# Performance work log

Hardware: AMD Instinct MI355X
Metric: run time of the kernel (lower is better)

## Reference

```python
import jax, jax.numpy as jnp
import numpy as np

DIM = 512        # model dim
MOE_DIM = 256    # expert hidden dim
E = 64           # n_routed experts
G = 8            # n_routed_group
TOPK_G = 4       # n_topk_group
K = 8            # n_experts_per_tok
SCALE = 2.5      # routed_scale
CAP = 1024


def setup_inputs() -> dict:
    key = jax.random.key(0)
    ks = jax.random.split(key, 6)
    x = jax.random.normal(ks[0], (4, 512, DIM), jnp.float32)
    gate_w = jax.random.normal(ks[1], (E, DIM), jnp.float32) / np.sqrt(DIM).astype(np.float32)
    gate_b = jax.random.normal(ks[2], (E,), jnp.float32) * 0.01
    w1 = jax.random.normal(ks[3], (E, DIM, MOE_DIM), jnp.float32) / np.sqrt(DIM).astype(np.float32)
    w3 = jax.random.normal(ks[4], (E, DIM, MOE_DIM), jnp.float32) / np.sqrt(DIM).astype(np.float32)
    w2 = jax.random.normal(ks[5], (E, MOE_DIM, DIM), jnp.float32) / np.sqrt(MOE_DIM).astype(np.float32)
    return {"x": x, "gate_w": gate_w, "gate_b": gate_b, "w1": w1, "w3": w3, "w2": w2}


def _gate(x2, gate_w, gate_b):
    # x2: [T, DIM] -> (weights [T,K], indices [T,K])
    T = x2.shape[0]
    scores = jax.nn.sigmoid(x2 @ gate_w.T)                      # [T, E]
    s = (scores + gate_b).reshape(T, G, E // G)                  # grouped scores
    group_scores = jax.lax.top_k(s, 2)[0].sum(-1)                # [T, G] sum of top-2 per group
    top_groups = jax.lax.top_k(group_scores, TOPK_G)[1]          # [T, TOPK_G]
    gmask = jnp.zeros((T, G), bool).at[jnp.arange(T)[:, None], top_groups].set(True)
    s = jnp.where(gmask[..., None], s, -jnp.inf).reshape(T, E)
    idx = jax.lax.top_k(s, K)[1]                                 # [T, K]
    w = jnp.take_along_axis(scores, idx, axis=1)                 # original (pre-bias) scores
    w = w / w.sum(-1, keepdims=True) * SCALE
    return w, idx


def _moe_forward(x, gate_w, gate_b, w1, w3, w2):
    shape = x.shape
    x2 = x.reshape(-1, DIM)                                      # [T, DIM]
    T = x2.shape[0]
    w, idx = _gate(x2, gate_w, gate_b)
    flat_e = idx.reshape(-1)                                     # [T*K]
    # position of each (token, slot) within its expert's buffer, in order
    oh = (flat_e[:, None] == jnp.arange(E)[None, :]).astype(jnp.int32)  # [T*K, E]
    pos = (jnp.cumsum(oh, axis=0) * oh).sum(-1) - 1              # [T*K]
    x_rep = jnp.repeat(x2, K, axis=0)                            # [T*K, DIM]
    # dispatch into per-expert buffers [E, CAP, DIM]
    xb = jnp.zeros((E, CAP, DIM), x2.dtype).at[flat_e, pos].set(x_rep, mode='drop')
    h = jax.nn.silu(jnp.einsum('ecd,edm->ecm', xb, w1)) * jnp.einsum('ecd,edm->ecm', xb, w3)
    yb = jnp.einsum('ecm,emd->ecd', h, w2)                       # [E, CAP, DIM]
    # combine: gather back and weight
    y = yb.at[flat_e, pos].get(mode='fill', fill_value=0.0) * w.reshape(-1)[:, None]
    return y.reshape(T, K, DIM).sum(1).reshape(shape)


def reference(x, gate_w, gate_b, w1, w3, w2):
    return _moe_forward(x, gate_w, gate_b, w1, w3, w2)
```

## Files before the change

kernel.cpp:

```cpp
#include <hip/hip_runtime.h>

#define T_TOK 2048
#define DIM   512
#define MOE   256
#define NE    64
#define NG    8
#define TOPKG 4
#define TOPK  8
#define CAP   1024
#define MOE_SCALE 2.5f

typedef float f32x4 __attribute__((ext_vector_type(4)));
typedef short s16x8 __attribute__((ext_vector_type(8)));

__device__ __forceinline__ unsigned short f2bf(float f) {
    unsigned u = __builtin_bit_cast(unsigned, f);
    unsigned r = (u + 0x7fffu + ((u >> 16) & 1u)) >> 16;
    return (unsigned short)r;
}
__device__ __forceinline__ unsigned pk2(float lo, float hi) {
    return (unsigned)f2bf(lo) | ((unsigned)f2bf(hi) << 16);
}

__device__ __forceinline__ void tile_scan(const int* __restrict__ counts, int lane,
                                          int e, int& G0, int& ne, int& nt)
{
    int cl = min(counts[lane], CAP);
    int ntl = (cl + 31) >> 5;
    int v = ntl;
#pragma unroll
    for (int d = 1; d < 64; d <<= 1) {
        int o = __shfl_up(v, d);
        if (lane >= d) v += o;
    }
    G0 = __shfl(v - ntl, e);
    ne = __shfl(cl, e);
    nt = __shfl(ntl, e);
}

__global__ __launch_bounds__(256) void gwt_k(const float* __restrict__ gw,
                                             float* __restrict__ gwT)
{
    int idx = blockIdx.x * 256 + threadIdx.x;
    int e = idx >> 9, k = idx & 511;
    gwT[(size_t)(k >> 2) * 256 + e * 4 + (k & 3)] = gw[idx];
}

__global__ __launch_bounds__(256) void gate_fused_k(const float* __restrict__ x,
                                                    const float* __restrict__ gwT,
                                                    const float* __restrict__ gb,
                                                    int* __restrict__ counts,
                                                    int* __restrict__ etok,
                                                    float* __restrict__ wt_of,
                                                    short* __restrict__ xb)
{
    __shared__ float xs[4][512];
    __shared__ float ps[4][4][64];
    int w = threadIdx.x >> 6, lane = threadIdx.x & 63;
    int t = blockIdx.x * 4 + w;

    {
        const float4* xr = (const float4*)(x + (size_t)t * DIM);
        float4 v0 = xr[lane * 2], v1 = xr[lane * 2 + 1];
        *(float4*)&xs[w][lane * 8]     = v0;
        *(float4*)&xs[w][lane * 8 + 4] = v1;
        short o[8];
        o[0] = (short)f2bf(v0.x); o[1] = (short)f2bf(v0.y);
        o[2] = (short)f2bf(v0.z); o[3] = (short)f2bf(v0.w);
        o[4] = (short)f2bf(v1.x); o[5] = (short)f2bf(v1.y);
        o[6] = (short)f2bf(v1.z); o[7] = (short)f2bf(v1.w);
        *(s16x8*)(xb + (size_t)t * DIM + lane * 8) = *(const s16x8*)o;
    }
    __syncthreads();

    const f32x4* gt = (const f32x4*)gwT;
    float a0 = 0.f, a1 = 0.f, a2 = 0.f, a3 = 0.f;
    int kb = w * 32;
#pragma unroll 8
    for (int k4 = 0; k4 < 32; ++k4) {
        f32x4 g  = gt[(size_t)(kb + k4) * 64 + lane];
        f32x4 x0 = *(const f32x4*)&xs[0][(kb + k4) * 4];
        f32x4 x1 = *(const f32x4*)&xs[1][(kb + k4) * 4];
        f32x4 x2 = *(const f32x4*)&xs[2][(kb + k4) * 4];
        f32x4 x3 = *(const f32x4*)&xs[3][(kb + k4) * 4];
        a0 += g.x * x0.x + g.y * x0.y + g.z * x0.z + g.w * x0.w;
        a1 += g.x * x1.x + g.y * x1.y + g.z * x1.z + g.w * x1.w;
        a2 += g.x * x2.x + g.y * x2.y + g.z * x2.z + g.w * x2.w;
        a3 += g.x * x3.x + g.y * x3.y + g.z * x3.z + g.w * x3.w;
    }
    ps[w][0][lane] = a0; ps[w][1][lane] = a1;
    ps[w][2][lane] = a2; ps[w][3][lane] = a3;
    __syncthreads();
    float acc = ps[0][w][lane] + ps[1][w][lane] + ps[2][w][lane] + ps[3][w][lane];

    float sc = 1.f / (1.f + __expf(-acc));
    float s  = sc + gb[lane];

    float m1 = s, m2 = -1e30f;
#pragma unroll
    for (int d = 1; d < 8; d <<= 1) {
        float o1 = __shfl_xor(m1, d);
        float o2 = __shfl_xor(m2, d);
        float n1 = fmaxf(m1, o1);
        float n2 = fmaxf(fminf(m1, o1), fmaxf(m2, o2));
        m1 = n1; m2 = n2;
    }
    float gv = m1 + m2;

    bool gkeep = false;
#pragma unroll
    for (int it = 0; it < TOPKG; ++it) {
        float m = gv;
#pragma unroll
        for (int d = 1; d < 64; d <<= 1) m = fmaxf(m, __shfl_xor(m, d));
        unsigned long long mask = __ballot(gv == m);
        int ldr = __ffsll(mask) - 1;
        if ((lane >> 3) == (ldr >> 3)) { gkeep = true; gv = -2e30f; }
    }
    float sv = gkeep ? s : -1e30f;

    float wsum = 0.f;
    int my_e = 0; float my_w = 0.f;
#pragma unroll
    for (int k = 0; k < TOPK; ++k) {
        float m = sv;
#pragma unroll
        for (int d = 1; d < 64; d <<= 1) m = fmaxf(m, __shfl_xor(m, d));
        unsigned long long mask = __ballot(sv == m);
        int l = __ffsll(mask) - 1;
        float wk = __shfl(sc, l);
        wsum += wk;
        if (lane == k) { my_e = l; my_w = wk; }
        if (lane == l) sv = -2e30f;
    }
    float scale = MOE_SCALE / wsum;
    if (lane < TOPK) {
        int p = atomicAdd(&counts[my_e], 1);
        int rid = t * TOPK + lane;
        bool ok = (p < CAP);
        if (ok) etok[my_e * CAP + p] = rid;
        wt_of[rid] = ok ? my_w * scale : 0.f;
    }
}

__global__ __launch_bounds__(256) void dispatch_k(const short* __restrict__ xb,
                                                  const int* __restrict__ counts,
                                                  const int* __restrict__ etok,
                                                  short* __restrict__ xg)
{
    int e = blockIdx.x & 63, sub = blockIdx.x >> 6;
    int w = threadIdx.x >> 6, lane = threadIdx.x & 63;

    int G0, ne, nt;
    tile_scan(counts, lane, e, G0, ne, nt);
    int rows = nt * 32;
    const int* el = etok + e * CAP;

    int kt = lane >> 2, qq = lane & 3;
    for (int p = sub * 4 + w; p < rows; p += 32) {
        s16x8 v = {0, 0, 0, 0, 0, 0, 0, 0};
        if (p < ne) {
            int tok = el[p] >> 3;
            v = *(const s16x8*)(xb + (size_t)tok * DIM + lane * 8);
        }
        int st = (p >> 4) & 1, m = p & 15;
        size_t off = ((((size_t)(G0 + (p >> 5)) * 16 + kt) * 2 + st) * 64
                      + (qq * 16 + m)) * 8;
        *(s16x8*)(xg + off) = v;
    }
}

__global__ __launch_bounds__(256, 3) void gemm1_k(const short* __restrict__ xg,
                                                  const float* __restrict__ w1,
                                                  const float* __restrict__ w3,
                                                  const int* __restrict__ counts,
                                                  short* __restrict__ hgf)
{
    __shared__ short Bl[2][16][64][8];
    __shared__ short Ct[4][2][16][24];

    int e  = blockIdx.x & 63, cg = blockIdx.x >> 6;
    int n0 = cg * 16;
    int tid = threadIdx.x;
    int w = tid >> 6, lane = tid & 63;
    int q = lane >> 4, m16 = lane & 15;

    int G0, ne, nt;
    tile_scan(counts, lane, e, G0, ne, nt);
    (void)ne;

    const float* W1e = w1 + (size_t)e * DIM * MOE + n0;
    const float* W3e = w3 + (size_t)e * DIM * MOE + n0;
#pragma unroll 4
    for (int it = 0; it < 8; ++it) {
        int idx = it * 256 + tid;
        int mat = idx >> 10;
        int rem = idx & 1023;
        int r2  = rem >> 2;
        int cq  = (rem & 3) * 4;
        int k   = r2 * 2;
        int kt = k >> 5, qf = (k >> 3) & 3, j0 = k & 7;
        const float* p = (mat ? W3e : W1e) + (size_t)k * MOE + cq;
        f32x4 lo = __builtin_nontemporal_load((const f32x4*)p);
        f32x4 hi = __builtin_nontemporal_load((const f32x4*)(p + MOE));
        unsigned* b = (unsigned*)&Bl[mat][kt][qf * 16 + cq][j0];
        b[0]  = pk2(lo.x, hi.x);
        b[4]  = pk2(lo.y, hi.y);
        b[8]  = pk2(lo.z, hi.z);
        b[12] = pk2(lo.w, hi.w);
    }
    __syncthreads();

    for (int T = w; T < nt; T += 4) {
        const short* A = xg + (size_t)(G0 + T) * 16384 + lane * 8;

        f32x4 acc[2][2];
#pragma unroll
        for (int i = 0; i < 2; ++i)
#pragma unroll
            for (int j = 0; j < 2; ++j) acc[i][j] = (f32x4)0.f;

        s16x8 pa0[2], pa1[2];
#pragma unroll
        for (int i = 0; i < 2; ++i) {
            pa0[i] = *(const s16x8*)(A + (i * 2 + 0) * 512);
            pa1[i] = *(const s16x8*)(A + (i * 2 + 1) * 512);
        }
#pragma unroll
        for (int kt = 0; kt < 16; ++kt) {
            s16x8 a0 = pa0[kt & 1], a1 = pa1[kt & 1];
            if (kt < 14) {
                pa0[kt & 1] = *(const s16x8*)(A + ((kt + 2) * 2 + 0) * 512);
                pa1[kt & 1] = *(const s16x8*)(A + ((kt + 2) * 2 + 1) * 512);
            }
            s16x8 b1 = *(const s16x8*)&Bl[0][kt][lane][0];
            s16x8 b3 = *(const s16x8*)&Bl[1][kt][lane][0];
            acc[0][0] = __builtin_amdgcn_mfma_f32_16x16x32_bf16(a0, b1, acc[0][0], 0, 0, 0);
            acc[1][0] = __builtin_amdgcn_mfma_f32_16x16x32_bf16(a1, b1, acc[1][0], 0, 0, 0);
            acc[0][1] = __builtin_amdgcn_mfma_f32_16x16x32_bf16(a0, b3, acc[0][1], 0, 0, 0);
            acc[1][1] = __builtin_amdgcn_mfma_f32_16x16x32_bf16(a1, b3, acc[1][1], 0, 0, 0);
        }

#pragma unroll
        for (int sub = 0; sub < 2; ++sub)
#pragma unroll
            for (int r = 0; r < 4; ++r) {
                float g = acc[sub][0][r];
                float u = acc[sub][1][r];
                float hv = g / (1.f + __expf(-g)) * u;
                Ct[w][sub][q * 4 + r][m16] = (short)f2bf(hv);
            }
        int subr = q >> 1;
        s16x8 hv8 = *(const s16x8*)&Ct[w][subr][m16][(q & 1) * 8];
        size_t slot = ((size_t)(G0 + T) * 8 + (cg >> 1)) * 2 + subr;
        *(s16x8*)(hgf + slot * 512 + ((cg & 1) * 2 + (q & 1)) * 128 + m16 * 8) = hv8;
    }
}

__global__ __launch_bounds__(256, 3) void gemm2_k(const short* __restrict__ hgf,
                                                  const float* __restrict__ w2,
                                                  const int* __restrict__ counts,
                                                  const int* __restrict__ etok,
                                                  short* __restrict__ ybuf)
{
    __shared__ short Bl[2][8][64][8];

    int e  = blockIdx.x & 63, cg = blockIdx.x >> 6;
    int n0 = cg * 32;
    int tid = threadIdx.x;
    int w = tid >> 6, lane = tid & 63;
    int q = lane >> 4, m16 = lane & 15;

    int G0, ne, nt;
    tile_scan(counts, lane, e, G0, ne, nt);

    const float* W2e = w2 + (size_t)e * MOE * DIM + n0;
#pragma unroll 4
    for (int it = 0; it < 4; ++it) {
        int idx = it * 256 + tid;
        int r2  = idx >> 3;
        int cq  = (idx & 7) * 4;
        int k   = r2 * 2;
        int kt2 = k >> 5, qf = (k >> 3) & 3, j0 = k & 7;
        int s = cq >> 4, c15 = cq & 15;
        const float* p = W2e + (size_t)k * DIM + cq;
        f32x4 lo = __builtin_nontemporal_load((const f32x4*)p);
        f32x4 hi = __builtin_nontemporal_load((const f32x4*)(p + DIM));
        unsigned* b = (unsigned*)&Bl[s][kt2][qf * 16 + c15][j0];
        b[0]  = pk2(lo.x, hi.x);
        b[4]  = pk2(lo.y, hi.y);
        b[8]  = pk2(lo.z, hi.z);
        b[12] = pk2(lo.w, hi.w);
    }
    __syncthreads();

    const int* el = etok + e * CAP;

    for (int T = w; T < nt; T += 4) {
        const short* A = hgf + (size_t)(G0 + T) * 8192 + lane * 8;

        int erid[2][4];
#pragma unroll
        for (int sub = 0; sub < 2; ++sub)
#pragma unroll
            for (int r = 0; r < 4; ++r) {
                int row = T * 32 + sub * 16 + q * 4 + r;
                erid[sub][r] = row < ne ? el[row] : -1;
            }

        f32x4 acc[2][2];
#pragma unroll
        for (int i = 0; i < 2; ++i)
#pragma unroll
            for (int j = 0; j < 2; ++j) acc[i][j] = (f32x4)0.f;

        s16x8 pa0[2], pa1[2];
#pragma unroll
        for (int i = 0; i < 2; ++i) {
            pa0[i] = *(const s16x8*)(A + (i * 2 + 0) * 512);
            pa1[i] = *(const s16x8*)(A + (i * 2 + 1) * 512);
        }
#pragma unroll
        for (int kt = 0; kt < 8; ++kt) {
            s16x8 a0 = pa0[kt & 1], a1 = pa1[kt & 1];
            if (kt < 6) {
                pa0[kt & 1] = *(const s16x8*)(A + ((kt + 2) * 2 + 0) * 512);
                pa1[kt & 1] = *(const s16x8*)(A + ((kt + 2) * 2 + 1) * 512);
            }
            s16x8 b0 = *(const s16x8*)&Bl[0][kt][lane][0];
            s16x8 b1 = *(const s16x8*)&Bl[1][kt][lane][0];
            acc[0][0] = __builtin_amdgcn_mfma_f32_16x16x32_bf16(a0, b0, acc[0][0], 0, 0, 0);
            acc[1][0] = __builtin_amdgcn_mfma_f32_16x16x32_bf16(a1, b0, acc[1][0], 0, 0, 0);
            acc[0][1] = __builtin_amdgcn_mfma_f32_16x16x32_bf16(a0, b1, acc[0][1], 0, 0, 0);
            acc[1][1] = __builtin_amdgcn_mfma_f32_16x16x32_bf16(a1, b1, acc[1][1], 0, 0, 0);
        }

#pragma unroll
        for (int sub = 0; sub < 2; ++sub)
#pragma unroll
            for (int s = 0; s < 2; ++s)
#pragma unroll
                for (int r = 0; r < 4; ++r) {
                    if (erid[sub][r] >= 0)
                        ybuf[(size_t)erid[sub][r] * DIM + n0 + s * 16 + m16] =
                            (short)f2bf(acc[sub][s][r]);
                }
    }
}

__global__ __launch_bounds__(256) void combine_k(const short* __restrict__ ybuf,
                                                 const float* __restrict__ wt_of,
                                                 float* __restrict__ out)
{
    int t = blockIdx.x;
    int tid = threadIdx.x;
    const int* yb = (const int*)ybuf;
    float sx = 0.f, sy = 0.f;
#pragma unroll
    for (int k = 0; k < TOPK; ++k) {
        float wk = wt_of[t * TOPK + k];
        int v = yb[(size_t)(t * TOPK + k) * (DIM / 2) + tid];
        float lo = __builtin_bit_cast(float, (unsigned)v << 16);
        float hi = __builtin_bit_cast(float, (unsigned)v & 0xffff0000u);
        sx += wk * lo;
        sy += wk * hi;
    }
    float2 o = {sx, sy};
    ((float2*)out)[(size_t)t * (DIM / 2) + tid] = o;
}

extern "C" void kernel_launch(void* const* d_in, const int* in_sizes, int n_in,
                              void* d_out, int out_size, void* d_ws, size_t ws_size,
                              hipStream_t stream)
{
    const float* x  = (const float*)d_in[0];
    const float* gw = (const float*)d_in[1];
    const float* gb = (const float*)d_in[2];
    const float* w1 = (const float*)d_in[3];
    const float* w3 = (const float*)d_in[4];
    const float* w2 = (const float*)d_in[5];

    char* ws = (char*)d_ws;
    short* xb    = (short*)(ws);
    short* hgf   = (short*)(ws + 2097152);
    short* xg    = (short*)(ws + 11534336);
    short* ybuf  = (short*)(ws + 11534336);
    float* gwT   = (float*)(ws + 30408704);
    int*   etok  = (int*)  (ws + 30539776);
    float* wt_of = (float*)(ws + 30801920);
    int*   counts= (int*)  (ws + 30867456);

    hipMemsetAsync(counts, 0, NE * 4, stream);

    gwt_k<<<128, 256, 0, stream>>>(gw, gwT);
    gate_fused_k<<<T_TOK / 4, 256, 0, stream>>>(x, gwT, gb, counts, etok, wt_of, xb);
    dispatch_k<<<NE * 8, 256, 0, stream>>>(xb, counts, etok, xg);
    gemm1_k<<<NE * 16, 256, 0, stream>>>(xg, w1, w3, counts, hgf);
    gemm2_k<<<NE * 16, 256, 0, stream>>>(hgf, w2, counts, etok, ybuf);
    combine_k<<<T_TOK, 256, 0, stream>>>(ybuf, wt_of, (float*)d_out);
}
```

Baseline: 244.1 us.

## Pre-pack expert weights to bf16 in extra blocks of gate and dispatch kernels

The fp32-to-bf16 conversion and LDS-layout packing of w1/w3 is moved into extra blocks of the gate kernel, and that of w2 into extra blocks of the dispatch kernel. Both write pre-swizzled bf16 buffers to workspace, and the GEMM kernels then only do straight 16-byte copies into LDS. The aim is to overlap weight conversion with the latency-bound gate and dispatch work and to halve the weight bytes the GEMMs read. The cost is an extra round trip of the packed weights through memory and a larger workspace.

```diff
diff --git a/kernel.cpp b/kernel.cpp
--- a/kernel.cpp
+++ b/kernel.cpp
@@ -46,17 +46,51 @@
     gwT[(size_t)(k >> 2) * 256 + e * 4 + (k & 3)] = gw[idx];
 }
 
-__global__ __launch_bounds__(256) void gate_fused_k(const float* __restrict__ x,
-                                                    const float* __restrict__ gwT,
-                                                    const float* __restrict__ gb,
-                                                    int* __restrict__ counts,
-                                                    int* __restrict__ etok,
-                                                    float* __restrict__ wt_of,
-                                                    short* __restrict__ xb)
+__global__ __launch_bounds__(256) void gate_pack_k(const float* __restrict__ x,
+                                                   const float* __restrict__ gwT,
+                                                   const float* __restrict__ gb,
+                                                   int* __restrict__ counts,
+                                                   int* __restrict__ etok,
+                                                   float* __restrict__ wt_of,
+                                                   short* __restrict__ xb,
+                                                   const float* __restrict__ w1,
+                                                   const float* __restrict__ w3,
+                                                   short* __restrict__ pw13)
 {
     __shared__ float xs[4][512];
     __shared__ float ps[4][4][64];
-    int w = threadIdx.x >> 6, lane = threadIdx.x & 63;
+    int tid = threadIdx.x;
+
+    if (blockIdx.x >= 512) {
+        int u = blockIdx.x - 512;
+        int e = u & 63, cg = u >> 6;
+        int n0 = cg * 16;
+        const float* W1e = w1 + (size_t)e * DIM * MOE + n0;
+        const float* W3e = w3 + (size_t)e * DIM * MOE + n0;
+        short* dst = pw13 + (size_t)(e * 16 + cg) * 16384;
+#pragma unroll 4
+        for (int it = 0; it < 8; ++it) {
+            int idx = it * 256 + tid;
+            int mat = idx >> 10;
+            int rem = idx & 1023;
+            int r2  = rem >> 2;
+            int cq  = (rem & 3) * 4;
+            int k   = r2 * 2;
+            int kt = k >> 5, qf = (k >> 3) & 3, j0 = k & 7;
+            const float* p = (mat ? W3e : W1e) + (size_t)k * MOE + cq;
+            f32x4 lo = *(const f32x4*)p;
+            f32x4 hi = *(const f32x4*)(p + MOE);
+            unsigned* b = (unsigned*)(dst +
+                (((mat * 16 + kt) * 64 + (qf * 16 + cq)) * 8 + j0));
+            b[0]  = pk2(lo.x, hi.x);
+            b[4]  = pk2(lo.y, hi.y);
+            b[8]  = pk2(lo.z, hi.z);
+            b[12] = pk2(lo.w, hi.w);
+        }
+        return;
+    }
+
+    int w = tid >> 6, lane = tid & 63;
     int t = blockIdx.x * 4 + w;
 
     {
@@ -143,13 +177,44 @@
     }
 }
 
-__global__ __launch_bounds__(256) void dispatch_k(const short* __restrict__ xb,
-                                                  const int* __restrict__ counts,
-                                                  const int* __restrict__ etok,
-                                                  short* __restrict__ xg)
-{
+__global__ __launch_bounds__(256) void dispatch_pack_k(const short* __restrict__ xb,
+                                                       const int* __restrict__ counts,
+                                                       const int* __restrict__ etok,
+                                                       short* __restrict__ xg,
+                                                       const float* __restrict__ w2,
+                                                       short* __restrict__ pw2)
+{
+    int tid = threadIdx.x;
+
+    if (blockIdx.x >= 512) {
+        int u = blockIdx.x - 512;
+        int e = u & 63, cg = u >> 6;
+        int n0 = cg * 32;
+        const float* W2e = w2 + (size_t)e * MOE * DIM + n0;
+        short* dst = pw2 + (size_t)(e * 16 + cg) * 8192;
+#pragma unroll 4
+        for (int it = 0; it < 4; ++it) {
+            int idx = it * 256 + tid;
+            int r2  = idx >> 3;
+            int cq  = (idx & 7) * 4;
+            int k   = r2 * 2;
+            int kt2 = k >> 5, qf = (k >> 3) & 3, j0 = k & 7;
+            int s = cq >> 4, c15 = cq & 15;
+            const float* p = W2e + (size_t)k * DIM + cq;
+            f32x4 lo = *(const f32x4*)p;
+            f32x4 hi = *(const f32x4*)(p + DIM);
+            unsigned* b = (unsigned*)(dst +
+                (((s * 8 + kt2) * 64 + (qf * 16 + c15)) * 8 + j0));
+            b[0]  = pk2(lo.x, hi.x);
+            b[4]  = pk2(lo.y, hi.y);
+            b[8]  = pk2(lo.z, hi.z);
+            b[12] = pk2(lo.w, hi.w);
+        }
+        return;
+    }
+
     int e = blockIdx.x & 63, sub = blockIdx.x >> 6;
-    int w = threadIdx.x >> 6, lane = threadIdx.x & 63;
+    int w = tid >> 6, lane = tid & 63;
 
     int G0, ne, nt;
     tile_scan(counts, lane, e, G0, ne, nt);
@@ -170,9 +235,8 @@
     }
 }
 
-__global__ __launch_bounds__(256, 3) void gemm1_k(const short* __restrict__ xg,
-                                                  const float* __restrict__ w1,
-                                                  const float* __restrict__ w3,
+__global__ __launch_bounds__(256, 3) void gemm1_k(const short* __restrict__ pw13,
+                                                  const short* __restrict__ xg,
                                                   const int* __restrict__ counts,
                                                   short* __restrict__ hgf)
 {
@@ -180,7 +244,6 @@
     __shared__ short Ct[4][2][16][24];
 
     int e  = blockIdx.x & 63, cg = blockIdx.x >> 6;
-    int n0 = cg * 16;
     int tid = threadIdx.x;
     int w = tid >> 6, lane = tid & 63;
     int q = lane >> 4, m16 = lane & 15;
@@ -189,25 +252,12 @@
     tile_scan(counts, lane, e, G0, ne, nt);
     (void)ne;
 
-    const float* W1e = w1 + (size_t)e * DIM * MOE + n0;
-    const float* W3e = w3 + (size_t)e * DIM * MOE + n0;
+    const short* src = pw13 + (size_t)(e * 16 + cg) * 16384;
+    short* dstl = &Bl[0][0][0][0];
 #pragma unroll 4
     for (int it = 0; it < 8; ++it) {
-        int idx = it * 256 + tid;
-        int mat = idx >> 10;
-        int rem = idx & 1023;
-        int r2  = rem >> 2;
-        int cq  = (rem & 3) * 4;
-        int k   = r2 * 2;
-        int kt = k >> 5, qf = (k >> 3) & 3, j0 = k & 7;
-        const float* p = (mat ? W3e : W1e) + (size_t)k * MOE + cq;
-        f32x4 lo = __builtin_nontemporal_load((const f32x4*)p);
-        f32x4 hi = __builtin_nontemporal_load((const f32x4*)(p + MOE));
-        unsigned* b = (unsigned*)&Bl[mat][kt][qf * 16 + cq][j0];
-        b[0]  = pk2(lo.x, hi.x);
-        b[4]  = pk2(lo.y, hi.y);
-        b[8]  = pk2(lo.z, hi.z);
-        b[12] = pk2(lo.w, hi.w);
+        int o = (it * 256 + tid) * 8;
+        *(s16x8*)(dstl + o) = *(const s16x8*)(src + o);
     }
     __syncthreads();
 
@@ -257,8 +307,8 @@
     }
 }
 
-__global__ __launch_bounds__(256, 3) void gemm2_k(const short* __restrict__ hgf,
-                                                  const float* __restrict__ w2,
+__global__ __launch_bounds__(256, 3) void gemm2_k(const short* __restrict__ pw2,
+                                                  const short* __restrict__ hgf,
                                                   const int* __restrict__ counts,
                                                   const int* __restrict__ etok,
                                                   short* __restrict__ ybuf)
@@ -274,23 +324,12 @@
     int G0, ne, nt;
     tile_scan(counts, lane, e, G0, ne, nt);
 
-    const float* W2e = w2 + (size_t)e * MOE * DIM + n0;
+    const short* src = pw2 + (size_t)(e * 16 + cg) * 8192;
+    short* dstl = &Bl[0][0][0][0];
 #pragma unroll 4
     for (int it = 0; it < 4; ++it) {
-        int idx = it * 256 + tid;
-        int r2  = idx >> 3;
-        int cq  = (idx & 7) * 4;
-        int k   = r2 * 2;
-        int kt2 = k >> 5, qf = (k >> 3) & 3, j0 = k & 7;
-        int s = cq >> 4, c15 = cq & 15;
-        const float* p = W2e + (size_t)k * DIM + cq;
-        f32x4 lo = __builtin_nontemporal_load((const f32x4*)p);
-        f32x4 hi = __builtin_nontemporal_load((const f32x4*)(p + DIM));
-        unsigned* b = (unsigned*)&Bl[s][kt2][qf * 16 + c15][j0];
-        b[0]  = pk2(lo.x, hi.x);
-        b[4]  = pk2(lo.y, hi.y);
-        b[8]  = pk2(lo.z, hi.z);
-        b[12] = pk2(lo.w, hi.w);
+        int o = (it * 256 + tid) * 8;
+        *(s16x8*)(dstl + o) = *(const s16x8*)(src + o);
     }
     __syncthreads();
 
@@ -384,18 +423,21 @@
     short* xb    = (short*)(ws);
     short* hgf   = (short*)(ws + 2097152);
     short* xg    = (short*)(ws + 11534336);
-    short* ybuf  = (short*)(ws + 11534336);
-    float* gwT   = (float*)(ws + 30408704);
-    int*   etok  = (int*)  (ws + 30539776);
-    float* wt_of = (float*)(ws + 30801920);
-    int*   counts= (int*)  (ws + 30867456);
+    short* pw13  = (short*)(ws + 30408704);
+    short* ybuf  = (short*)(ws + 30408704);
+    short* pw2   = (short*)(ws + 63963136);
+    float* gwT   = (float*)(ws + 80740352);
+    int*   etok  = (int*)  (ws + 80871424);
+    float* wt_of = (float*)(ws + 81133568);
+    int*   counts= (int*)  (ws + 81199104);
 
     hipMemsetAsync(counts, 0, NE * 4, stream);
 
     gwt_k<<<128, 256, 0, stream>>>(gw, gwT);
-    gate_fused_k<<<T_TOK / 4, 256, 0, stream>>>(x, gwT, gb, counts, etok, wt_of, xb);
-    dispatch_k<<<NE * 8, 256, 0, stream>>>(xb, counts, etok, xg);
-    gemm1_k<<<NE * 16, 256, 0, stream>>>(xg, w1, w3, counts, hgf);
-    gemm2_k<<<NE * 16, 256, 0, stream>>>(hgf, w2, counts, etok, ybuf);
+    gate_pack_k<<<1536, 256, 0, stream>>>(x, gwT, gb, counts, etok, wt_of, xb,
+                                          w1, w3, pw13);
+    dispatch_pack_k<<<1536, 256, 0, stream>>>(xb, counts, etok, xg, w2, pw2);
+    gemm1_k<<<NE * 16, 256, 0, stream>>>(pw13, xg, counts, hgf);
+    gemm2_k<<<NE * 16, 256, 0, stream>>>(pw2, hgf, counts, etok, ybuf);
     combine_k<<<T_TOK, 256, 0, stream>>>(ybuf, wt_of, (float*)d_out);
 }
```

After: 257.5 us. 5.5% more time.
